# Performance work log

Measured on AMD Instinct MI355X. Metric: run time of the kernel, lower is better.

The kernel has to match this reference:

```python
import jax, jax.numpy as jnp
import numpy as np

B, S, D = 16, 2048, 128

def setup_inputs() -> dict:
    key = jax.random.key(0)
    k1, k2, k3 = jax.random.split(key, 3)
    return {
        "query": jax.random.normal(k1, (B, S, D), dtype=jnp.float32),
        "key": jax.random.normal(k2, (B, S, D), dtype=jnp.float32),
        "value": jax.random.normal(k3, (B, S, D), dtype=jnp.float32),
    }

def reference(query, key, value):
    dq = query.shape[-1]
    dk = key.shape[-1]
    # custom scale: sqrt(Dq) + sqrt(Dk - Dq); with Dq == Dk this is sqrt(Dq)
    inv_scale = np.sqrt(dq) + np.sqrt(dk - dq)
    qk = jnp.einsum("bqd,bkd->bqk", query, key) / jnp.float32(inv_scale)
    attn = jax.nn.softmax(qk, axis=-1)  # dropout_p=0 -> identity
    return jnp.einsum("bqk,bkd->bqd", attn, value)
```

## Files before the change

kernel.cpp:

```cpp
#include <hip/hip_runtime.h>
#include <stdint.h>

#define Bn 16
#define Sn 2048
#define Dn 128
#define QBLK 128
#define KVBLK 64
#define NTHR 512
#define NT (Sn / KVBLK)

typedef __attribute__((ext_vector_type(4))) float f32x4;
typedef __attribute__((ext_vector_type(16))) float f32x16;
typedef __attribute__((ext_vector_type(8))) short bf16x8;
typedef __attribute__((ext_vector_type(2))) unsigned int u32x2;

#define BUFSZ 32768
#define SMEM_BYTES 67584

__device__ __forceinline__ uint32_t f2bf_u(float f) {
  return (__float_as_uint(f) + 0x8000u) >> 16;
}
__device__ __forceinline__ uint32_t pk2(float a, float b) {
  return f2bf_u(a) | (f2bf_u(b) << 16);
}

__global__ __launch_bounds__(256) void tr_kv(const float* __restrict__ K,
                                             const float* __restrict__ V,
                                             unsigned short* __restrict__ Kf,
                                             unsigned short* __restrict__ Vf) {
  __shared__ unsigned short lds[64 * 136];
  const int tid = threadIdx.x;
  const size_t tileoff = (size_t)blockIdx.x * (64 * Dn);

  {
    const float* src = K + tileoff;
#pragma unroll
    for (int it = 0; it < 8; ++it) {
      const int gr = it * 256 + tid;
      const int k = gr >> 5, g4 = gr & 31;
      const float4 v = ((const float4*)src)[gr];
      unsigned short* p = &lds[k * 136 + g4 * 4];
      p[0] = (unsigned short)f2bf_u(v.x);
      p[1] = (unsigned short)f2bf_u(v.y);
      p[2] = (unsigned short)f2bf_u(v.z);
      p[3] = (unsigned short)f2bf_u(v.w);
    }
    __syncthreads();
    char* dst = (char*)Kf + (size_t)blockIdx.x * 16384;
#pragma unroll
    for (int it = 0; it < 4; ++it) {
      const int g = it * 256 + tid;
      const int lane = g & 63, dk = (g >> 6) & 7, h = g >> 9;
      const unsigned short* p =
          &lds[(32 * h + (lane & 31)) * 136 + dk * 16 + 8 * (lane >> 5)];
      uint4 o;
      o.x = (uint32_t)p[0] | ((uint32_t)p[1] << 16);
      o.y = (uint32_t)p[2] | ((uint32_t)p[3] << 16);
      o.z = (uint32_t)p[4] | ((uint32_t)p[5] << 16);
      o.w = (uint32_t)p[6] | ((uint32_t)p[7] << 16);
      *(uint4*)(dst + g * 16) = o;
    }
  }
  __syncthreads();

  {
    const float* src = V + tileoff;
#pragma unroll
    for (int it = 0; it < 8; ++it) {
      const int gr = it * 256 + tid;
      const int k = gr >> 5, g4 = gr & 31;
      const float4 v = ((const float4*)src)[gr];
      unsigned short* p = &lds[k * 136 + g4 * 4];
      p[0] = (unsigned short)f2bf_u(v.x);
      p[1] = (unsigned short)f2bf_u(v.y);
      p[2] = (unsigned short)f2bf_u(v.z);
      p[3] = (unsigned short)f2bf_u(v.w);
    }
    __syncthreads();
    char* dst = (char*)Vf + (size_t)blockIdx.x * 16384;
#pragma unroll
    for (int it = 0; it < 4; ++it) {
      const int g = it * 256 + tid;
      const int lane = g & 63, f3 = (g >> 6) & 7, h = g >> 9;
      const int d = (f3 >> 1) * 32 + (lane & 31);
      const int k0 = 32 * h + (f3 & 1) * 16 + 8 * (lane >> 5);
      uint4 o;
      o.x = (uint32_t)lds[(k0 + 0) * 136 + d] | ((uint32_t)lds[(k0 + 1) * 136 + d] << 16);
      o.y = (uint32_t)lds[(k0 + 2) * 136 + d] | ((uint32_t)lds[(k0 + 3) * 136 + d] << 16);
      o.z = (uint32_t)lds[(k0 + 4) * 136 + d] | ((uint32_t)lds[(k0 + 5) * 136 + d] << 16);
      o.w = (uint32_t)lds[(k0 + 6) * 136 + d] | ((uint32_t)lds[(k0 + 7) * 136 + d] << 16);
      *(uint4*)(dst + g * 16) = o;
    }
  }
}

__global__ __launch_bounds__(NTHR, 2) void attn_fwd(
    const float* __restrict__ Q, const unsigned short* __restrict__ Kf,
    const unsigned short* __restrict__ Vf, float* __restrict__ O) {
  __shared__ uint4 smem_[SMEM_BYTES / 16];
  char* smem = (char*)smem_;

  const int tid = threadIdx.x;
  const int lane = tid & 63;
  const int w = tid >> 6;
  const int qw = w & 3;
  const int h = w >> 2;
  const int hi = lane >> 5;
  const int ql = lane & 31;

  const int i = blockIdx.x;
  const int j = i >> 3;
  const int b = (i & 7) + 8 * (j & 1);
  const int q0 = (j >> 1) * QBLK;
  const int qg = q0 + qw * 32 + ql;

  const float qscale = 0.08838834764831845f * 1.44269504088896340736f;
  bf16x8 qf[8];
  {
    const float* qrow = Q + (size_t)(b * Sn + qg) * Dn;
#pragma unroll
    for (int dk = 0; dk < 8; ++dk) {
      const int d0 = dk * 16 + hi * 8;
      const float4 a = *(const float4*)(qrow + d0);
      const float4 d = *(const float4*)(qrow + d0 + 4);
      bf16x8 q8;
      q8[0] = (short)f2bf_u(a.x * qscale); q8[1] = (short)f2bf_u(a.y * qscale);
      q8[2] = (short)f2bf_u(a.z * qscale); q8[3] = (short)f2bf_u(a.w * qscale);
      q8[4] = (short)f2bf_u(d.x * qscale); q8[5] = (short)f2bf_u(d.y * qscale);
      q8[6] = (short)f2bf_u(d.z * qscale); q8[7] = (short)f2bf_u(d.w * qscale);
      qf[dk] = q8;
    }
  }

  f32x16 o[4];
#pragma unroll
  for (int dt = 0; dt < 4; ++dt) {
#pragma unroll
    for (int jj = 0; jj < 16; ++jj) o[dt][jj] = 0.f;
  }
  float l_r = 0.f;

  const char* Kg = (const char*)(Kf + (size_t)b * Sn * Dn);
  const char* Vg = (const char*)(Vf + (size_t)b * Sn * Dn);

#define STAGE(dst_, t_)                                                        \
  {                                                                            \
    const char* gk = Kg + (size_t)(t_)*16384 + w * 2048 + lane * 16;           \
    const char* gv = Vg + (size_t)(t_)*16384 + w * 2048 + lane * 16;           \
    char* lk = smem + (dst_) + w * 2048;                                       \
    char* lv = smem + (dst_) + 16384 + w * 2048;                               \
    _Pragma("unroll") for (int it = 0; it < 2; ++it) {                         \
      __builtin_amdgcn_global_load_lds(                                        \
          (const __attribute__((address_space(1))) uint32_t*)(gk + it * 1024), \
          (__attribute__((address_space(3))) uint32_t*)(lk + it * 1024),       \
          16, 0, 0);                                                           \
      __builtin_amdgcn_global_load_lds(                                        \
          (const __attribute__((address_space(1))) uint32_t*)(gv + it * 1024), \
          (__attribute__((address_space(3))) uint32_t*)(lv + it * 1024),       \
          16, 0, 0);                                                           \
    }                                                                          \
  }

#define TILE(cb_)                                                              \
  {                                                                            \
    bf16x8 vfr[8];                                                             \
    {                                                                          \
      const char* vt = smem + (cb_) + 16384 + h * 8192 + lane * 16;            \
      _Pragma("unroll") for (int f = 0; f < 8; ++f)                            \
          vfr[f] = *(const bf16x8*)(vt + f * 1024);                            \
    }                                                                          \
    f32x16 s;                                                                  \
    _Pragma("unroll") for (int jj = 0; jj < 16; ++jj) s[jj] = -8.0f;           \
    {                                                                          \
      const char* kt = smem + (cb_) + h * 8192 + lane * 16;                    \
      __builtin_amdgcn_s_setprio(1);                                           \
      _Pragma("unroll") for (int dk = 0; dk < 8; ++dk) {                       \
        bf16x8 kfr = *(const bf16x8*)(kt + dk * 1024);                         \
        s = __builtin_amdgcn_mfma_f32_32x32x16_bf16(kfr, qf[dk], s, 0, 0, 0);  \
      }                                                                        \
      __builtin_amdgcn_s_setprio(0);                                           \
    }                                                                          \
    _Pragma("unroll") for (int jj = 0; jj < 16; ++jj)                          \
        s[jj] = __builtin_amdgcn_exp2f(s[jj]);                                 \
    {                                                                          \
      float r0 = 0.f, r1 = 0.f, r2 = 0.f, r3 = 0.f;                            \
      _Pragma("unroll") for (int jj = 0; jj < 4; ++jj) {                       \
        r0 += s[jj]; r1 += s[4 + jj]; r2 += s[8 + jj]; r3 += s[12 + jj];       \
      }                                                                        \
      l_r += (r0 + r1) + (r2 + r3);      \
    }                                                                          \
    uint32_t own[4][2];                                                        \
    _Pragma("unroll") for (int mm = 0; mm < 4; ++mm) {                         \
      own[mm][0] = pk2(s[4 * mm + 0], s[4 * mm + 1]);                          \
      own[mm][1] = pk2(s[4 * mm + 2], s[4 * mm + 3]);                          \
    }                                                                          \
    uint32_t rcv[2][2];                                                        \
    _Pragma("unroll") for (int jj = 0; jj < 2; ++jj)                           \
        _Pragma("unroll") for (int e = 0; e < 2; ++e) {                        \
      uint32_t sel = hi ? own[2 * jj][e] : own[2 * jj + 1][e];                 \
      rcv[jj][e] = (uint32_t)__shfl_xor((int)sel, 32, 64);                     \
    }                                                                          \
    bf16x8 pb[2];                                                              \
    _Pragma("unroll") for (int ks = 0; ks < 2; ++ks) {                         \
      union { uint32_t u[4]; bf16x8 v; } tt;                                   \
      tt.u[0] = hi ? rcv[ks][0] : own[2 * ks][0];                              \
      tt.u[1] = hi ? rcv[ks][1] : own[2 * ks][1];                              \
      tt.u[2] = hi ? own[2 * ks + 1][0] : rcv[ks][0];                          \
      tt.u[3] = hi ? own[2 * ks + 1][1] : rcv[ks][1];                          \
      pb[ks] = tt.v;                                                           \
    }                                                                          \
    __builtin_amdgcn_s_setprio(1);                                             \
    _Pragma("unroll") for (int dt = 0; dt < 4; ++dt) {                         \
      _Pragma("unroll") for (int ks = 0; ks < 2; ++ks) {                       \
        o[dt] = __builtin_amdgcn_mfma_f32_32x32x16_bf16(vfr[dt * 2 + ks],      \
                                                        pb[ks], o[dt], 0, 0, 0);\
      }                                                                        \
    }                                                                          \
    __builtin_amdgcn_s_setprio(0);                                             \
  }

  STAGE(0, 0)
  __syncthreads();
  for (int t = 0; t < NT; ++t) {
    const uint32_t cb = (uint32_t)(t & 1) * BUFSZ;
    if (t + 1 < NT) STAGE(BUFSZ - cb, t + 1)
    __builtin_amdgcn_sched_barrier(0);
    TILE(cb)
    __syncthreads();
  }

  l_r += __shfl_xor(l_r, 32, 64);
  char* xch = smem + qw * 16896;
  if (h) {
#pragma unroll
    for (int dt = 0; dt < 4; ++dt) {
#pragma unroll
      for (int q2 = 0; q2 < 4; ++q2) {
        float4 v;
        v.x = o[dt][4 * q2 + 0]; v.y = o[dt][4 * q2 + 1];
        v.z = o[dt][4 * q2 + 2]; v.w = o[dt][4 * q2 + 3];
        *(float4*)(xch + (dt * 4 + q2) * 1024 + lane * 16) = v;
      }
    }
    *(float*)(xch + 16384 + lane * 4) = l_r;
  }
  __syncthreads();
  if (!h) {
    const float l1 = *(const float*)(xch + 16384 + lane * 4);
    const float inv = 1.0f / (l_r + l1);
    float* orow = O + (size_t)(b * Sn + qg) * Dn;
#pragma unroll
    for (int dt = 0; dt < 4; ++dt) {
#pragma unroll
      for (int q2 = 0; q2 < 4; ++q2) {
        const float4 o1v =
            *(const float4*)(xch + (dt * 4 + q2) * 1024 + lane * 16);
        float4 v;
        v.x = (o[dt][4 * q2 + 0] + o1v.x) * inv;
        v.y = (o[dt][4 * q2 + 1] + o1v.y) * inv;
        v.z = (o[dt][4 * q2 + 2] + o1v.z) * inv;
        v.w = (o[dt][4 * q2 + 3] + o1v.w) * inv;
        *(float4*)(orow + dt * 32 + q2 * 8 + hi * 4) = v;
      }
    }
  }
}

extern "C" void kernel_launch(void* const* d_in, const int* in_sizes, int n_in,
                              void* d_out, int out_size, void* d_ws, size_t ws_size,
                              hipStream_t stream) {
  (void)in_sizes; (void)n_in; (void)out_size; (void)ws_size;
  const float* Q = (const float*)d_in[0];
  const float* K = (const float*)d_in[1];
  const float* V = (const float*)d_in[2];
  float* O = (float*)d_out;

  const size_t nE = (size_t)Bn * Sn * Dn;
  unsigned short* Kf = (unsigned short*)d_ws;
  unsigned short* Vf = Kf + nE;

  tr_kv<<<dim3(Bn * 32, 1, 1), dim3(256, 1, 1), 0, stream>>>(K, V, Kf, Vf);
  attn_fwd<<<dim3((Sn / QBLK) * Bn, 1, 1), dim3(NTHR, 1, 1), 0, stream>>>(
      Q, Kf, Vf, O);
}
```

Measured before the change: 58.71 us.

## Software-pipeline QK^T of next KV tile with softmax and PV of current

Splits the per-tile body into separate V-fragment load, QK^T MFMA, and softmax+PV stages. The loop is unrolled by two with ping-pong score accumulators, so the next tile's QK^T MFMAs are issued before the current tile's exp/pack/PV work. V fragments are pulled into registers before the barrier, which lets the next async stage overwrite that buffer early. The aim is to overlap MFMA work with the exp and shuffle ALU work and hide LDS latency. The cost is another 16-float accumulator live, which raises register pressure, and the removed sched_barrier leaves instruction ordering to the compiler.

```diff
diff --git a/kernel.cpp b/kernel.cpp
--- a/kernel.cpp
+++ b/kernel.cpp
@@ -161,38 +161,40 @@
     }                                                                          \
   }
 
-#define TILE(cb_)                                                              \
-  {                                                                            \
-    bf16x8 vfr[8];                                                             \
-    {                                                                          \
-      const char* vt = smem + (cb_) + 16384 + h * 8192 + lane * 16;            \
-      _Pragma("unroll") for (int f = 0; f < 8; ++f)                            \
-          vfr[f] = *(const bf16x8*)(vt + f * 1024);                            \
-    }                                                                          \
-    f32x16 s;                                                                  \
-    _Pragma("unroll") for (int jj = 0; jj < 16; ++jj) s[jj] = -8.0f;           \
-    {                                                                          \
-      const char* kt = smem + (cb_) + h * 8192 + lane * 16;                    \
-      __builtin_amdgcn_s_setprio(1);                                           \
-      _Pragma("unroll") for (int dk = 0; dk < 8; ++dk) {                       \
-        bf16x8 kfr = *(const bf16x8*)(kt + dk * 1024);                         \
-        s = __builtin_amdgcn_mfma_f32_32x32x16_bf16(kfr, qf[dk], s, 0, 0, 0);  \
-      }                                                                        \
-      __builtin_amdgcn_s_setprio(0);                                           \
-    }                                                                          \
+#define LOADVF(vd_, cb_)                                                       \
+  {                                                                            \
+    const char* vt = smem + (cb_) + 16384 + h * 8192 + lane * 16;              \
+    _Pragma("unroll") for (int f = 0; f < 8; ++f)                              \
+        vd_[f] = *(const bf16x8*)(vt + f * 1024);                              \
+  }
+
+#define QKT(sd_, cb_)                                                          \
+  {                                                                            \
+    _Pragma("unroll") for (int jj = 0; jj < 16; ++jj) sd_[jj] = -8.0f;         \
+    const char* kt = smem + (cb_) + h * 8192 + lane * 16;                      \
+    __builtin_amdgcn_s_setprio(1);                                             \
+    _Pragma("unroll") for (int dk = 0; dk < 8; ++dk) {                         \
+      bf16x8 kfr = *(const bf16x8*)(kt + dk * 1024);                           \
+      sd_ = __builtin_amdgcn_mfma_f32_32x32x16_bf16(kfr, qf[dk], sd_, 0, 0, 0);\
+    }                                                                          \
+    __builtin_amdgcn_s_setprio(0);                                             \
+  }
+
+#define SOFTPV(s_, vf_)                                                        \
+  {                                                                            \
     _Pragma("unroll") for (int jj = 0; jj < 16; ++jj)                          \
-        s[jj] = __builtin_amdgcn_exp2f(s[jj]);                                 \
+        s_[jj] = __builtin_amdgcn_exp2f(s_[jj]);                               \
     {                                                                          \
       float r0 = 0.f, r1 = 0.f, r2 = 0.f, r3 = 0.f;                            \
       _Pragma("unroll") for (int jj = 0; jj < 4; ++jj) {                       \
-        r0 += s[jj]; r1 += s[4 + jj]; r2 += s[8 + jj]; r3 += s[12 + jj];       \
+        r0 += s_[jj]; r1 += s_[4 + jj]; r2 += s_[8 + jj]; r3 += s_[12 + jj];   \
       }                                                                        \
       l_r += (r0 + r1) + (r2 + r3);      \
     }                                                                          \
     uint32_t own[4][2];                                                        \
     _Pragma("unroll") for (int mm = 0; mm < 4; ++mm) {                         \
-      own[mm][0] = pk2(s[4 * mm + 0], s[4 * mm + 1]);                          \
-      own[mm][1] = pk2(s[4 * mm + 2], s[4 * mm + 3]);                          \
+      own[mm][0] = pk2(s_[4 * mm + 0], s_[4 * mm + 1]);                        \
+      own[mm][1] = pk2(s_[4 * mm + 2], s_[4 * mm + 3]);                        \
     }                                                                          \
     uint32_t rcv[2][2];                                                        \
     _Pragma("unroll") for (int jj = 0; jj < 2; ++jj)                           \
@@ -212,21 +214,30 @@
     __builtin_amdgcn_s_setprio(1);                                             \
     _Pragma("unroll") for (int dt = 0; dt < 4; ++dt) {                         \
       _Pragma("unroll") for (int ks = 0; ks < 2; ++ks) {                       \
-        o[dt] = __builtin_amdgcn_mfma_f32_32x32x16_bf16(vfr[dt * 2 + ks],      \
+        o[dt] = __builtin_amdgcn_mfma_f32_32x32x16_bf16(vf_[dt * 2 + ks],      \
                                                         pb[ks], o[dt], 0, 0, 0);\
       }                                                                        \
     }                                                                          \
     __builtin_amdgcn_s_setprio(0);                                             \
   }
 
+  bf16x8 vA[8];
+  f32x16 sA, sB;
   STAGE(0, 0)
   __syncthreads();
-  for (int t = 0; t < NT; ++t) {
-    const uint32_t cb = (uint32_t)(t & 1) * BUFSZ;
-    if (t + 1 < NT) STAGE(BUFSZ - cb, t + 1)
-    __builtin_amdgcn_sched_barrier(0);
-    TILE(cb)
-    __syncthreads();
+  STAGE(BUFSZ, 1)
+  QKT(sA, 0)
+  for (int t = 0; t < NT; t += 2) {
+    LOADVF(vA, 0)
+    __syncthreads();
+    if (t + 2 < NT) STAGE(0, t + 2)
+    if (t + 1 < NT) QKT(sB, BUFSZ)
+    SOFTPV(sA, vA)
+    LOADVF(vA, BUFSZ)
+    __syncthreads();
+    if (t + 3 < NT) STAGE(BUFSZ, t + 3)
+    if (t + 2 < NT) QKT(sA, 0)
+    SOFTPV(sB, vA)
   }
 
   l_r += __shfl_xor(l_r, 32, 64);
```

Result: no change. 58.30 us (-0.7%).
